# Kernel tuning notes

Hardware: AMD Instinct MI355X
Metric: run time of the kernel (lower is better)

## Reference

```python
import jax, jax.numpy as jnp
import numpy as np

N_NODES = 50000
N_EDGES = 800000
N_FEAT = 256
HIDDEN = 64
N_CLASSES = 16
T_END = 3.0  # opt['time']; rk4 takes one step over [0, 3]


def spline_conv(x, src, dst, p, W, R, b, n):
    """SplineConv, dim=1, kernel_size=2, degree=1 open B-spline, aggr='mean'.
    x: [n, Cin]; src/dst: [E]; p: [E,1] pseudo-coords in [0,1];
    W: [2, Cin, Cout]; R: [Cin, Cout]; b: [Cout]."""
    xj = x[src]  # gather source node features [E, Cin]
    # basis weights for K=2, degree=1: (1-p) on kernel 0, p on kernel 1
    msg = ((1.0 - p) * xj) @ W[0] + (p * xj) @ W[1]  # [E, Cout]
    agg = jax.ops.segment_sum(msg, dst, num_segments=n)
    deg = jax.ops.segment_sum(jnp.ones((msg.shape[0], 1), msg.dtype), dst, num_segments=n)
    return agg / jnp.maximum(deg, 1.0) + x @ R + b


def setup_inputs() -> dict:
    key = jax.random.key(0)
    ks = jax.random.split(key, 20)
    x = jax.random.normal(ks[0], (N_NODES, N_FEAT), jnp.float32)
    edge_attr = jax.random.uniform(ks[1], (N_EDGES, 1), jnp.float32)
    src = jax.random.randint(ks[2], (N_EDGES,), 0, N_NODES)
    dst = jax.random.randint(ks[3], (N_EDGES,), 0, N_NODES)

    def w(k, shape, fan_in):
        s = 1.0 / np.sqrt(fan_in)
        return jax.random.uniform(k, shape, jnp.float32, -s, s)

    # conv1: num_features -> hidden
    W1 = w(ks[4], (2, N_FEAT, HIDDEN), N_FEAT)
    R1 = w(ks[5], (N_FEAT, HIDDEN), N_FEAT)
    b1 = jnp.zeros((HIDDEN,), jnp.float32)
    # ODE func: two stacked SplineConvs hidden -> hidden
    Wa = w(ks[6], (2, HIDDEN, HIDDEN), HIDDEN)
    Ra = w(ks[7], (HIDDEN, HIDDEN), HIDDEN)
    ba = jnp.zeros((HIDDEN,), jnp.float32)
    Wb = w(ks[8], (2, HIDDEN, HIDDEN), HIDDEN)
    Rb = w(ks[9], (HIDDEN, HIDDEN), HIDDEN)
    bb = jnp.zeros((HIDDEN,), jnp.float32)
    # conv2: hidden -> num_classes
    W2 = w(ks[10], (2, HIDDEN, N_CLASSES), HIDDEN)
    R2 = w(ks[11], (HIDDEN, N_CLASSES), HIDDEN)
    b2 = jnp.zeros((N_CLASSES,), jnp.float32)

    return dict(x=x, edge_attr=edge_attr, src=src, dst=dst,
                W1=W1, R1=R1, b1=b1, Wa=Wa, Ra=Ra, ba=ba,
                Wb=Wb, Rb=Rb, bb=bb, W2=W2, R2=R2, b2=b2)


def reference(x, edge_attr, src, dst, W1, R1, b1, Wa, Ra, ba, Wb, Rb, bb, W2, R2, b2):
    n = x.shape[0]
    p = edge_attr
    h = jnp.tanh(spline_conv(x, src, dst, p, W1, R1, b1, n))
    # dropout is identity in eval mode

    def f(y):  # GCNLayer: two stacked SplineConvs, no activation
        y = spline_conv(y, src, dst, p, Wa, Ra, ba, n)
        return spline_conv(y, src, dst, p, Wb, Rb, bb, n)

    # single RK4 step from t=0 to t=T_END (torchdiffeq fixed-grid rk4 on s_span=[0,3])
    k1 = f(h)
    k2 = f(h + 0.5 * T_END * k1)
    k3 = f(h + 0.5 * T_END * k2)
    k4 = f(h + T_END * k3)
    h = h + (T_END / 6.0) * (k1 + 2.0 * k2 + 2.0 * k3 + k4)

    out = jnp.tanh(spline_conv(h, src, dst, p, W2, R2, b2, n))
    return jax.nn.log_softmax(out, axis=1)
```

## Files before the change

### kernel.cpp

```cpp
#include <hip/hip_runtime.h>
#include <math.h>

static inline int ceil_div(int a, int b) { return (a + b - 1) / b; }


__global__ __launch_bounds__(256) void zero2(int* __restrict__ a, int* __restrict__ b,
                                             int n) {
    int i = blockIdx.x * 256 + threadIdx.x;
    if (i < n) { a[i] = 0; b[i] = 0; }
}

__global__ __launch_bounds__(256) void hist_kernel(const int* __restrict__ dst,
                                                   int* __restrict__ deg, int E) {
    int e = blockIdx.x * 256 + threadIdx.x;
    if (e < E) atomicAdd(&deg[dst[e]], 1);
}

__global__ __launch_bounds__(256) void scan_blocksum(const int* __restrict__ deg,
                                                     int* __restrict__ bsum, int n) {
    __shared__ int red[256];
    int t = threadIdx.x;
    int base = blockIdx.x * 2048 + t * 8;
    int s = 0;
    #pragma unroll
    for (int i = 0; i < 8; ++i) {
        int idx = base + i;
        if (idx < n) s += deg[idx];
    }
    red[t] = s;
    __syncthreads();
    #pragma unroll
    for (int off = 128; off >= 1; off >>= 1) {
        if (t < off) red[t] += red[t + off];
        __syncthreads();
    }
    if (t == 0) bsum[blockIdx.x] = red[0];
}

__global__ __launch_bounds__(256) void scan_tops(int* __restrict__ bsum, int nb) {
    __shared__ int sh[256];
    int t = threadIdx.x;
    int orig = (t < nb) ? bsum[t] : 0;
    sh[t] = orig;
    __syncthreads();
    for (int off = 1; off < 256; off <<= 1) {
        int add = (t >= off) ? sh[t - off] : 0;
        __syncthreads();
        sh[t] += add;
        __syncthreads();
    }
    if (t < nb) bsum[t] = sh[t] - orig;
}

__global__ __launch_bounds__(256) void scan_final(const int* __restrict__ deg,
                                                  const int* __restrict__ bsum,
                                                  int* __restrict__ rowp,
                                                  float* __restrict__ invd,
                                                  int n, int E) {
    __shared__ int sh[256];
    int t = threadIdx.x;
    int base = blockIdx.x * 2048 + t * 8;
    int loc[8];
    int s = 0;
    #pragma unroll
    for (int i = 0; i < 8; ++i) {
        int idx = base + i;
        int d = (idx < n) ? deg[idx] : 0;
        loc[i] = d;
        s += d;
    }
    sh[t] = s;
    __syncthreads();
    for (int off = 1; off < 256; off <<= 1) {
        int add = (t >= off) ? sh[t - off] : 0;
        __syncthreads();
        sh[t] += add;
        __syncthreads();
    }
    int run = bsum[blockIdx.x] + (sh[t] - s);
    #pragma unroll
    for (int i = 0; i < 8; ++i) {
        int idx = base + i;
        if (idx < n) {
            rowp[idx] = run;
            int d = loc[i];
            run += d;
            invd[idx] = 1.0f / (float)(d > 1 ? d : 1);
        }
    }
    if (blockIdx.x == 0 && t == 0) rowp[n] = E;
}

__global__ __launch_bounds__(256) void scatter_idx(const int* __restrict__ dst,
                                                   const int* __restrict__ rowp,
                                                   int* __restrict__ fill,
                                                   int* __restrict__ ei, int E) {
    int e = blockIdx.x * 256 + threadIdx.x;
    if (e >= E) return;
    int d = dst[e];
    int pos = rowp[d] + atomicAdd(&fill[d], 1);
    ei[pos] = e;
}

__global__ __launch_bounds__(256) void sort_fill(const int* __restrict__ rowp,
                                                 int* __restrict__ ei,
                                                 const int* __restrict__ src,
                                                 const float* __restrict__ p,
                                                 int2* __restrict__ epk, int n) {
    int node = blockIdx.x * 256 + threadIdx.x;
    if (node >= n) return;
    int b = rowp[node], e = rowp[node + 1];
    for (int i = b + 1; i < e; ++i) {
        int key = ei[i];
        int j = i - 1;
        while (j >= b && ei[j] > key) { ei[j + 1] = ei[j]; --j; }
        ei[j + 1] = key;
    }
    for (int i = b; i < e; ++i) {
        int id = ei[i];
        epk[i] = make_int2(src[id], __float_as_int(p[id]));
    }
}

__global__ __launch_bounds__(256) void pack_all(
    const float* __restrict__ W1, const float* __restrict__ R1,
    const float* __restrict__ Wa, const float* __restrict__ Ra,
    const float* __restrict__ Wb, const float* __restrict__ Rb,
    const float* __restrict__ W2, const float* __restrict__ R2,
    float* __restrict__ Bc1, float* __restrict__ Bca,
    float* __restrict__ Bcb, float* __restrict__ Bc2) {
    int idx = blockIdx.x * 256 + threadIdx.x;
    const int S1 = 256 * 192, S2 = 192 * 64, S4 = 64 * 48;
    if (idx < S1) {
        int k = idx / 192, c = idx % 192;
        float v;
        if (c < 64)       v = W1[k * 64 + c];
        else if (c < 128) v = W1[256 * 64 + k * 64 + (c - 64)];
        else              v = R1[k * 64 + (c - 128)];
        Bc1[idx] = v;
        return;
    }
    idx -= S1;
    if (idx < S2) { Bca[idx] = (idx < 8192) ? Wa[idx] : Ra[idx - 8192]; return; }
    idx -= S2;
    if (idx < S2) { Bcb[idx] = (idx < 8192) ? Wb[idx] : Rb[idx - 8192]; return; }
    idx -= S2;
    if (idx < S4) {
        int k = idx / 48, c = idx % 48;
        float v;
        if (c < 16)      v = W2[k * 16 + c];
        else if (c < 32) v = W2[64 * 16 + k * 16 + (c - 16)];
        else             v = R2[k * 16 + (c - 32)];
        Bc2[idx] = v;
    }
}

__global__ __launch_bounds__(256) void edge_agg64_v5(const float* __restrict__ x,
                                                     const int* __restrict__ rowp,
                                                     const int2* __restrict__ epk,
                                                     const float* __restrict__ invd,
                                                     float* __restrict__ agg, int n) {
    int gid = blockIdx.x * 256 + threadIdx.x;
    int node = gid >> 4;
    if (node >= n) return;
    int c4 = (gid & 15) << 2;
    int e = rowp[node], eend = rowp[node + 1];
    float sx = 0.f, sy = 0.f, sz = 0.f, sw = 0.f;
    float px = 0.f, py = 0.f, pz = 0.f, pw = 0.f;
    for (; e + 4 <= eend; e += 4) {
        int2 q0 = epk[e], q1 = epk[e + 1], q2 = epk[e + 2], q3 = epk[e + 3];
        int s0 = q0.x, s1 = q1.x, s2 = q2.x, s3 = q3.x;
        float p0 = __int_as_float(q0.y), p1 = __int_as_float(q1.y);
        float p2 = __int_as_float(q2.y), p3 = __int_as_float(q3.y);
        float4 v0 = *reinterpret_cast<const float4*>(&x[(size_t)s0 * 64 + c4]);
        float4 v1 = *reinterpret_cast<const float4*>(&x[(size_t)s1 * 64 + c4]);
        float4 v2 = *reinterpret_cast<const float4*>(&x[(size_t)s2 * 64 + c4]);
        float4 v3 = *reinterpret_cast<const float4*>(&x[(size_t)s3 * 64 + c4]);
        sx += (v0.x + v1.x) + (v2.x + v3.x);
        sy += (v0.y + v1.y) + (v2.y + v3.y);
        sz += (v0.z + v1.z) + (v2.z + v3.z);
        sw += (v0.w + v1.w) + (v2.w + v3.w);
        px = fmaf(p0, v0.x, fmaf(p1, v1.x, fmaf(p2, v2.x, fmaf(p3, v3.x, px))));
        py = fmaf(p0, v0.y, fmaf(p1, v1.y, fmaf(p2, v2.y, fmaf(p3, v3.y, py))));
        pz = fmaf(p0, v0.z, fmaf(p1, v1.z, fmaf(p2, v2.z, fmaf(p3, v3.z, pz))));
        pw = fmaf(p0, v0.w, fmaf(p1, v1.w, fmaf(p2, v2.w, fmaf(p3, v3.w, pw))));
    }
    for (; e < eend; ++e) {
        int2 q = epk[e];
        int s = q.x;
        float pe = __int_as_float(q.y);
        float4 v = *reinterpret_cast<const float4*>(&x[(size_t)s * 64 + c4]);
        sx += v.x; sy += v.y; sz += v.z; sw += v.w;
        px = fmaf(pe, v.x, px); py = fmaf(pe, v.y, py);
        pz = fmaf(pe, v.z, pz); pw = fmaf(pe, v.w, pw);
    }
    float w = invd[node];
    float4 a0 = make_float4((sx - px) * w, (sy - py) * w, (sz - pz) * w, (sw - pw) * w);
    float4 a1 = make_float4(px * w, py * w, pz * w, pw * w);
    *reinterpret_cast<float4*>(&agg[(size_t)node * 128 + c4]) = a0;
    *reinterpret_cast<float4*>(&agg[(size_t)node * 128 + 64 + c4]) = a1;
}

__global__ __launch_bounds__(256) void hidden_gemm_db(
    const float* __restrict__ agg, const float* __restrict__ in,
    const float* __restrict__ B, const float* __restrict__ bias,
    int n, int mode, float* __restrict__ u_out,
    const float* __restrict__ hbuf, const float* __restrict__ acc_in,
    float* __restrict__ acc_out, float* __restrict__ t_out,
    float c1, float c2, float c3) {
    __shared__ __align__(16) float As[2][16][68];
    __shared__ __align__(16) float Bs[2][16][68];
    const int t = threadIdx.x;
    const int row0 = blockIdx.x * 64;
    const int ty = t >> 4, tx = t & 15;
    const int lrow = t >> 2, lk = (t & 3) << 2;
    const int bkk = t >> 4, bcol = (t & 15) << 2;

    float4 av = make_float4(0.f, 0.f, 0.f, 0.f);
    {
        int r = row0 + lrow;
        if (r < n) av = *reinterpret_cast<const float4*>(&agg[(size_t)r * 128 + lk]);
    }
    float4 bv = *reinterpret_cast<const float4*>(&B[(size_t)bkk * 64 + bcol]);
    As[0][lk + 0][lrow] = av.x; As[0][lk + 1][lrow] = av.y;
    As[0][lk + 2][lrow] = av.z; As[0][lk + 3][lrow] = av.w;
    *reinterpret_cast<float4*>(&Bs[0][bkk][bcol]) = bv;
    __syncthreads();

    float acc[4][4];
    #pragma unroll
    for (int i = 0; i < 4; ++i)
        #pragma unroll
        for (int j = 0; j < 4; ++j) acc[i][j] = 0.f;

    for (int kt = 0; kt < 12; ++kt) {
        const int cur = kt & 1;
        if (kt + 1 < 12) {
            int k0 = (kt + 1) << 4;
            int r = row0 + lrow;
            int kk = k0 + lk;
            av = make_float4(0.f, 0.f, 0.f, 0.f);
            if (r < n)
                av = (kk < 128)
                    ? *reinterpret_cast<const float4*>(&agg[(size_t)r * 128 + kk])
                    : *reinterpret_cast<const float4*>(&in[(size_t)r * 64 + (kk - 128)]);
            bv = *reinterpret_cast<const float4*>(&B[(size_t)(k0 + bkk) * 64 + bcol]);
        }
        #pragma unroll
        for (int kk = 0; kk < 16; ++kk) {
            float4 a4 = *reinterpret_cast<const float4*>(&As[cur][kk][ty << 2]);
            float4 b4 = *reinterpret_cast<const float4*>(&Bs[cur][kk][tx << 2]);
            float aa[4] = {a4.x, a4.y, a4.z, a4.w};
            float bb[4] = {b4.x, b4.y, b4.z, b4.w};
            #pragma unroll
            for (int i = 0; i < 4; ++i)
                #pragma unroll
                for (int j = 0; j < 4; ++j)
                    acc[i][j] = fmaf(aa[i], bb[j], acc[i][j]);
        }
        if (kt + 1 < 12) {
            const int nx = cur ^ 1;
            As[nx][lk + 0][lrow] = av.x; As[nx][lk + 1][lrow] = av.y;
            As[nx][lk + 2][lrow] = av.z; As[nx][lk + 3][lrow] = av.w;
            *reinterpret_cast<float4*>(&Bs[nx][bkk][bcol]) = bv;
        }
        __syncthreads();
    }

    float4 bia = *reinterpret_cast<const float4*>(&bias[tx << 2]);
    #pragma unroll
    for (int i = 0; i < 4; ++i) {
        int r = row0 + (ty << 2) + i;
        if (r >= n) continue;
        size_t idx = (size_t)r * 64 + (tx << 2);
        float4 v = make_float4(acc[i][0] + bia.x, acc[i][1] + bia.y,
                               acc[i][2] + bia.z, acc[i][3] + bia.w);
        if (mode == 0) {
            *reinterpret_cast<float4*>(&u_out[idx]) = v;
        } else {
            float4 ai = make_float4(0.f, 0.f, 0.f, 0.f);
            if (acc_in) ai = *reinterpret_cast<const float4*>(&acc_in[idx]);
            float4 an = make_float4(ai.x + c3 * v.x, ai.y + c3 * v.y,
                                    ai.z + c3 * v.z, ai.w + c3 * v.w);
            *reinterpret_cast<float4*>(&acc_out[idx]) = an;
            float4 hb = *reinterpret_cast<const float4*>(&hbuf[idx]);
            float4 to = make_float4(hb.x + c1 * v.x + c2 * an.x,
                                    hb.y + c1 * v.y + c2 * an.y,
                                    hb.z + c1 * v.z + c2 * an.z,
                                    hb.w + c1 * v.w + c2 * an.w);
            *reinterpret_cast<float4*>(&t_out[idx]) = to;
        }
    }
}

__global__ __launch_bounds__(128) void conv1_gemm_v5(const float* __restrict__ x,
                                                     const float* __restrict__ B,
                                                     int n, float* __restrict__ yz,
                                                     float* __restrict__ base,
                                                     const float* __restrict__ b1) {
    __shared__ __align__(16) float As[16][36];
    __shared__ __align__(16) float Bs[16][200];
    const int t = threadIdx.x;
    const int row0 = blockIdx.x * 32;
    const int ty = t >> 4, tx = t & 15;
    const int arow = t >> 2, alk = (t & 3) << 2;
    const int bkk0 = t >> 4, bcol = (t & 15) << 2;
    float acc[4][12];
    #pragma unroll
    for (int i = 0; i < 4; ++i)
        #pragma unroll
        for (int j = 0; j < 12; ++j) acc[i][j] = 0.f;

    for (int kt = 0; kt < 16; ++kt) {
        int k0 = kt << 4;
        {
            float4 av = make_float4(0.f, 0.f, 0.f, 0.f);
            int r = row0 + arow;
            if (r < n)
                av = *reinterpret_cast<const float4*>(&x[(size_t)r * 256 + k0 + alk]);
            As[alk + 0][arow] = av.x; As[alk + 1][arow] = av.y;
            As[alk + 2][arow] = av.z; As[alk + 3][arow] = av.w;
        }
        #pragma unroll
        for (int hh = 0; hh < 2; ++hh) {
            int kk = bkk0 + 8 * hh;
            const float* bp = &B[(size_t)(k0 + kk) * 192 + bcol];
            *reinterpret_cast<float4*>(&Bs[kk][bcol])       = *reinterpret_cast<const float4*>(bp);
            *reinterpret_cast<float4*>(&Bs[kk][bcol + 64])  = *reinterpret_cast<const float4*>(bp + 64);
            *reinterpret_cast<float4*>(&Bs[kk][bcol + 128]) = *reinterpret_cast<const float4*>(bp + 128);
        }
        __syncthreads();
        #pragma unroll
        for (int kk = 0; kk < 16; ++kk) {
            float4 a0 = *reinterpret_cast<const float4*>(&As[kk][ty << 2]);
            float4 b0 = *reinterpret_cast<const float4*>(&Bs[kk][tx << 2]);
            float4 b1q = *reinterpret_cast<const float4*>(&Bs[kk][(tx << 2) + 64]);
            float4 b2q = *reinterpret_cast<const float4*>(&Bs[kk][(tx << 2) + 128]);
            float aa[4] = {a0.x, a0.y, a0.z, a0.w};
            float bb[12] = {b0.x, b0.y, b0.z, b0.w, b1q.x, b1q.y, b1q.z, b1q.w,
                            b2q.x, b2q.y, b2q.z, b2q.w};
            #pragma unroll
            for (int i = 0; i < 4; ++i)
                #pragma unroll
                for (int j = 0; j < 12; ++j)
                    acc[i][j] = fmaf(aa[i], bb[j], acc[i][j]);
        }
        __syncthreads();
    }

    float4 bb4 = *reinterpret_cast<const float4*>(&b1[tx << 2]);
    #pragma unroll
    for (int i = 0; i < 4; ++i) {
        int r = row0 + (ty << 2) + i;
        if (r >= n) continue;
        float4 q0 = make_float4(acc[i][0], acc[i][1], acc[i][2], acc[i][3]);
        float4 q1 = make_float4(acc[i][4], acc[i][5], acc[i][6], acc[i][7]);
        float4 q2 = make_float4(acc[i][8] + bb4.x, acc[i][9] + bb4.y,
                                acc[i][10] + bb4.z, acc[i][11] + bb4.w);
        *reinterpret_cast<float4*>(&yz[(size_t)r * 128 + (tx << 2)]) = q0;
        *reinterpret_cast<float4*>(&yz[(size_t)r * 128 + 64 + (tx << 2)]) = q1;
        *reinterpret_cast<float4*>(&base[(size_t)r * 64 + (tx << 2)]) = q2;
    }
}

__global__ __launch_bounds__(256) void edge_tf64_v8(const float* __restrict__ yz,
                                                    const int* __restrict__ rowp,
                                                    const int2* __restrict__ epk,
                                                    const float* __restrict__ invd,
                                                    const float* __restrict__ base,
                                                    float* __restrict__ out, int n) {
    int gid = blockIdx.x * 256 + threadIdx.x;
    int node = gid >> 3;
    if (node >= n) return;
    int c8 = (gid & 7) << 3;
    int e = rowp[node], eend = rowp[node + 1];
    float a[8] = {0.f, 0.f, 0.f, 0.f, 0.f, 0.f, 0.f, 0.f};
    for (; e + 2 <= eend; e += 2) {
        int2 q0 = epk[e], q1 = epk[e + 1];
        int s0 = q0.x, s1 = q1.x;
        float p0 = __int_as_float(q0.y), p1 = __int_as_float(q1.y);
        float4 y0a = *reinterpret_cast<const float4*>(&yz[(size_t)s0 * 128 + c8]);
        float4 y0b = *reinterpret_cast<const float4*>(&yz[(size_t)s0 * 128 + c8 + 4]);
        float4 z0a = *reinterpret_cast<const float4*>(&yz[(size_t)s0 * 128 + 64 + c8]);
        float4 z0b = *reinterpret_cast<const float4*>(&yz[(size_t)s0 * 128 + 64 + c8 + 4]);
        float4 y1a = *reinterpret_cast<const float4*>(&yz[(size_t)s1 * 128 + c8]);
        float4 y1b = *reinterpret_cast<const float4*>(&yz[(size_t)s1 * 128 + c8 + 4]);
        float4 z1a = *reinterpret_cast<const float4*>(&yz[(size_t)s1 * 128 + 64 + c8]);
        float4 z1b = *reinterpret_cast<const float4*>(&yz[(size_t)s1 * 128 + 64 + c8 + 4]);
        const float* ya0 = &y0a.x; const float* yb0 = &y0b.x;
        const float* za0 = &z0a.x; const float* zb0 = &z0b.x;
        const float* ya1 = &y1a.x; const float* yb1 = &y1b.x;
        const float* za1 = &z1a.x; const float* zb1 = &z1b.x;
        #pragma unroll
        for (int j = 0; j < 4; ++j) {
            a[j]     += fmaf(p0, za0[j] - ya0[j], ya0[j]) + fmaf(p1, za1[j] - ya1[j], ya1[j]);
            a[4 + j] += fmaf(p0, zb0[j] - yb0[j], yb0[j]) + fmaf(p1, zb1[j] - yb1[j], yb1[j]);
        }
    }
    for (; e < eend; ++e) {
        int2 q = epk[e];
        int s = q.x;
        float pe = __int_as_float(q.y);
        float4 ya = *reinterpret_cast<const float4*>(&yz[(size_t)s * 128 + c8]);
        float4 yb = *reinterpret_cast<const float4*>(&yz[(size_t)s * 128 + c8 + 4]);
        float4 za = *reinterpret_cast<const float4*>(&yz[(size_t)s * 128 + 64 + c8]);
        float4 zb = *reinterpret_cast<const float4*>(&yz[(size_t)s * 128 + 64 + c8 + 4]);
        const float* fy = &ya.x; const float* gy = &yb.x;
        const float* fz = &za.x; const float* gz = &zb.x;
        #pragma unroll
        for (int j = 0; j < 4; ++j) {
            a[j]     += fmaf(pe, fz[j] - fy[j], fy[j]);
            a[4 + j] += fmaf(pe, gz[j] - gy[j], gy[j]);
        }
    }
    float w = invd[node];
    size_t idx = (size_t)node * 64 + c8;
    float4 ba = *reinterpret_cast<const float4*>(&base[idx]);
    float4 bbv = *reinterpret_cast<const float4*>(&base[idx + 4]);
    float4 o0 = make_float4(tanhf(fmaf(a[0], w, ba.x)), tanhf(fmaf(a[1], w, ba.y)),
                            tanhf(fmaf(a[2], w, ba.z)), tanhf(fmaf(a[3], w, ba.w)));
    float4 o1 = make_float4(tanhf(fmaf(a[4], w, bbv.x)), tanhf(fmaf(a[5], w, bbv.y)),
                            tanhf(fmaf(a[6], w, bbv.z)), tanhf(fmaf(a[7], w, bbv.w)));
    *reinterpret_cast<float4*>(&out[idx]) = o0;
    *reinterpret_cast<float4*>(&out[idx + 4]) = o1;
}

__global__ __launch_bounds__(256) void edge_tf16_lsm(const float* __restrict__ yz,
                                                     const int* __restrict__ rowp,
                                                     const int2* __restrict__ epk,
                                                     const float* __restrict__ invd,
                                                     const float* __restrict__ base,
                                                     float* __restrict__ out, int n) {
    int gid = blockIdx.x * 256 + threadIdx.x;
    int node = gid >> 4;
    if (node >= n) return;
    int c = gid & 15;
    int e = rowp[node], eend = rowp[node + 1];
    float a = 0.f;
    for (; e + 4 <= eend; e += 4) {
        int2 q0 = epk[e], q1 = epk[e + 1], q2 = epk[e + 2], q3 = epk[e + 3];
        int s0 = q0.x, s1 = q1.x, s2 = q2.x, s3 = q3.x;
        float p0 = __int_as_float(q0.y), p1 = __int_as_float(q1.y);
        float p2 = __int_as_float(q2.y), p3 = __int_as_float(q3.y);
        float y0 = yz[(size_t)s0 * 32 + c],      z0 = yz[(size_t)s0 * 32 + 16 + c];
        float y1 = yz[(size_t)s1 * 32 + c],      z1 = yz[(size_t)s1 * 32 + 16 + c];
        float y2 = yz[(size_t)s2 * 32 + c],      z2 = yz[(size_t)s2 * 32 + 16 + c];
        float y3 = yz[(size_t)s3 * 32 + c],      z3 = yz[(size_t)s3 * 32 + 16 + c];
        a += fmaf(p0, z0 - y0, y0);
        a += fmaf(p1, z1 - y1, y1);
        a += fmaf(p2, z2 - y2, y2);
        a += fmaf(p3, z3 - y3, y3);
    }
    for (; e < eend; ++e) {
        int2 q = epk[e];
        int s = q.x; float pe = __int_as_float(q.y);
        float y = yz[(size_t)s * 32 + c], z = yz[(size_t)s * 32 + 16 + c];
        a += fmaf(pe, z - y, y);
    }
    float o = tanhf(a * invd[node] + base[(size_t)node * 16 + c]);
    float m = o;
    #pragma unroll
    for (int off = 8; off >= 1; off >>= 1) m = fmaxf(m, __shfl_xor(m, off, 16));
    float ex = expf(o - m);
    float s = ex;
    #pragma unroll
    for (int off = 8; off >= 1; off >>= 1) s += __shfl_xor(s, off, 16);
    out[(size_t)node * 16 + c] = (o - m) - logf(s);
}

__global__ __launch_bounds__(256) void gemm_tiled(
    const float* __restrict__ A0, int lda0, int K0,
    const float* __restrict__ A1, int lda1,
    const float* __restrict__ B,
    int n, int K, int M,
    float* __restrict__ out0, int w0, const float* __restrict__ bias0,
    float* __restrict__ out1, int w1, const float* __restrict__ bias1,
    int split) {
    __shared__ __align__(16) float As[16][68];
    __shared__ __align__(16) float Bs[16][68];
    const int t = threadIdx.x;
    const int row0 = blockIdx.x * 64;
    const int col0 = blockIdx.y * 64;
    const int ty = t >> 4, tx = t & 15;
    const int lrow = t >> 2, lk = (t & 3) << 2;
    const int bkk = t >> 4, bcol = (t & 15) << 2;
    float acc[4][4];
    #pragma unroll
    for (int i = 0; i < 4; ++i)
        #pragma unroll
        for (int j = 0; j < 4; ++j) acc[i][j] = 0.f;

    for (int k0 = 0; k0 < K; k0 += 16) {
        float4 av = make_float4(0.f, 0.f, 0.f, 0.f);
        {
            int r = row0 + lrow;
            if (r < n) {
                int kk = k0 + lk;
                const float* src = (kk < K0)
                    ? (A0 + (size_t)r * lda0 + kk)
                    : (A1 + (size_t)r * lda1 + (kk - K0));
                av = *reinterpret_cast<const float4*>(src);
            }
        }
        float4 bv = make_float4(0.f, 0.f, 0.f, 0.f);
        {
            int c = col0 + bcol;
            int kk = k0 + bkk;
            if (c < M) bv = *reinterpret_cast<const float4*>(B + (size_t)kk * M + c);
        }
        As[lk + 0][lrow] = av.x; As[lk + 1][lrow] = av.y;
        As[lk + 2][lrow] = av.z; As[lk + 3][lrow] = av.w;
        *reinterpret_cast<float4*>(&Bs[bkk][bcol]) = bv;
        __syncthreads();
        #pragma unroll
        for (int kk = 0; kk < 16; ++kk) {
            float4 a4 = *reinterpret_cast<const float4*>(&As[kk][ty << 2]);
            float4 b4 = *reinterpret_cast<const float4*>(&Bs[kk][tx << 2]);
            float aa[4] = {a4.x, a4.y, a4.z, a4.w};
            float bb[4] = {b4.x, b4.y, b4.z, b4.w};
            #pragma unroll
            for (int i = 0; i < 4; ++i)
                #pragma unroll
                for (int j = 0; j < 4; ++j)
                    acc[i][j] = fmaf(aa[i], bb[j], acc[i][j]);
        }
        __syncthreads();
    }

    #pragma unroll
    for (int i = 0; i < 4; ++i) {
        int r = row0 + (ty << 2) + i;
        if (r >= n) continue;
        #pragma unroll
        for (int j = 0; j < 4; ++j) {
            int c = col0 + (tx << 2) + j;
            if (c >= M) continue;
            float v = acc[i][j];
            if (c < split) {
                if (bias0) v += bias0[c];
                out0[(size_t)r * w0 + c] = v;
            } else {
                int cc = c - split;
                if (bias1) v += bias1[cc];
                out1[(size_t)r * w1 + cc] = v;
            }
        }
    }
}


static void hidden_conv(hipStream_t stream, const float* in, float* agg,
                        const int* rowp, const int2* epk,
                        const float* invd, const float* Bc, const float* bias, int n,
                        int mode, float* u_out,
                        const float* h, const float* acc_in, float* acc_out,
                        float* t_out, float c1, float c2, float c3) {
    edge_agg64_v5<<<ceil_div(n * 16, 256), 256, 0, stream>>>(in, rowp, epk, invd,
                                                             agg, n);
    hidden_gemm_db<<<ceil_div(n, 64), 256, 0, stream>>>(agg, in, Bc, bias, n, mode,
                                                        u_out, h, acc_in, acc_out,
                                                        t_out, c1, c2, c3);
}

extern "C" void kernel_launch(void* const* d_in, const int* in_sizes, int n_in,
                              void* d_out, int out_size, void* d_ws, size_t ws_size,
                              hipStream_t stream) {
    const float* x  = (const float*)d_in[0];
    const float* pE = (const float*)d_in[1];
    const int*   sr = (const int*)d_in[2];
    const int*   ds = (const int*)d_in[3];
    const float* W1 = (const float*)d_in[4];
    const float* R1 = (const float*)d_in[5];
    const float* b1 = (const float*)d_in[6];
    const float* Wa = (const float*)d_in[7];
    const float* Ra = (const float*)d_in[8];
    const float* ba = (const float*)d_in[9];
    const float* Wb = (const float*)d_in[10];
    const float* Rb = (const float*)d_in[11];
    const float* bb = (const float*)d_in[12];
    const float* W2 = (const float*)d_in[13];
    const float* R2 = (const float*)d_in[14];
    const float* b2 = (const float*)d_in[15];
    const int n = in_sizes[0] / 256;
    const int E = in_sizes[2];
    float* out = (float*)d_out;

    char* w = (char*)d_ws;
    auto alloc = [&](size_t bytes) -> void* {
        void* ptr = (void*)w;
        w += (bytes + 255) & ~(size_t)255;
        return ptr;
    };
    int nscan = ceil_div(n, 2048);
    int*   deg  = (int*)alloc((size_t)n * 4);
    int*   fill = (int*)alloc((size_t)n * 4);
    int*   rowp = (int*)alloc((size_t)(n + 1) * 4);
    float* invd = (float*)alloc((size_t)n * 4);
    int*   bsum = (int*)alloc((size_t)256 * 4);
    int*   ei   = (int*)alloc((size_t)E * 4);
    int2*  epk  = (int2*)alloc((size_t)E * 8);
    float* Bc1  = (float*)alloc((size_t)256 * 192 * 4);
    float* Bca  = (float*)alloc((size_t)192 * 64 * 4);
    float* Bcb  = (float*)alloc((size_t)192 * 64 * 4);
    float* Bc2  = (float*)alloc((size_t)64 * 48 * 4);
    float* big0 = (float*)alloc((size_t)n * 128 * 4);
    float* big1 = (float*)alloc((size_t)n * 64 * 4);
    float* h    = (float*)alloc((size_t)n * 64 * 4);
    float* u    = (float*)alloc((size_t)n * 64 * 4);
    float* tb   = (float*)alloc((size_t)n * 64 * 4);
    float* acc  = (float*)alloc((size_t)n * 64 * 4);

    const int PACK_TOTAL = 256 * 192 + 2 * 192 * 64 + 64 * 48;

    zero2<<<ceil_div(n, 256), 256, 0, stream>>>(deg, fill, n);
    pack_all<<<ceil_div(PACK_TOTAL, 256), 256, 0, stream>>>(W1, R1, Wa, Ra, Wb, Rb,
                                                            W2, R2, Bc1, Bca, Bcb, Bc2);
    hist_kernel<<<ceil_div(E, 256), 256, 0, stream>>>(ds, deg, E);
    scan_blocksum<<<nscan, 256, 0, stream>>>(deg, bsum, n);
    scan_tops<<<1, 256, 0, stream>>>(bsum, nscan);
    scan_final<<<nscan, 256, 0, stream>>>(deg, bsum, rowp, invd, n, E);
    scatter_idx<<<ceil_div(E, 256), 256, 0, stream>>>(ds, rowp, fill, ei, E);
    sort_fill<<<ceil_div(n, 256), 256, 0, stream>>>(rowp, ei, sr, pE, epk, n);

    conv1_gemm_v5<<<ceil_div(n, 32), 128, 0, stream>>>(x, Bc1, n, big0, big1, b1);
    edge_tf64_v8<<<ceil_div(n * 8, 256), 256, 0, stream>>>(big0, rowp, epk, invd,
                                                           big1, h, n);

    hidden_conv(stream, h, big0, rowp, epk, invd, Bca, ba, n, 0, u,
                nullptr, nullptr, nullptr, nullptr, 0.f, 0.f, 0.f);
    hidden_conv(stream, u, big0, rowp, epk, invd, Bcb, bb, n, 1, nullptr,
                h, nullptr, acc, tb, 1.5f, 0.f, 1.f);
    hidden_conv(stream, tb, big0, rowp, epk, invd, Bca, ba, n, 0, u,
                nullptr, nullptr, nullptr, nullptr, 0.f, 0.f, 0.f);
    hidden_conv(stream, u, big0, rowp, epk, invd, Bcb, bb, n, 1, nullptr,
                h, acc, acc, tb, 1.5f, 0.f, 2.f);
    hidden_conv(stream, tb, big0, rowp, epk, invd, Bca, ba, n, 0, u,
                nullptr, nullptr, nullptr, nullptr, 0.f, 0.f, 0.f);
    hidden_conv(stream, u, big0, rowp, epk, invd, Bcb, bb, n, 1, nullptr,
                h, acc, acc, tb, 3.f, 0.f, 2.f);
    hidden_conv(stream, tb, big0, rowp, epk, invd, Bca, ba, n, 0, u,
                nullptr, nullptr, nullptr, nullptr, 0.f, 0.f, 0.f);
    hidden_conv(stream, u, big0, rowp, epk, invd, Bcb, bb, n, 1, nullptr,
                h, acc, acc, tb, 0.f, 0.5f, 1.f);

    gemm_tiled<<<dim3(ceil_div(n, 64), 1), 256, 0, stream>>>(
        tb, 64, 64, nullptr, 0, Bc2, n, 64, 48,
        big0, 32, nullptr, big1, 16, b2, 32);
    edge_tf16_lsm<<<ceil_div(n * 16, 256), 256, 0, stream>>>(big0, rowp, epk, invd,
                                                             big1, out, n);
}
```

Measured before the change: 894.9 us.

## Fuse hidden-layer edge aggregation into GEMM kernel via shared-memory staging

Merges the separate edge-aggregation kernel and the hidden GEMM into one kernel. Each block first gathers neighbour features for its 64 nodes, writing the transposed aggregates into shared memory, then runs the GEMM against those and the self features. This removes the global write and re-read of the 128-wide aggregate buffer and one launch per conv, and unrolls the gather loop to 8 edges. In exchange the GEMM loses its double buffering, shared memory per block grows (about 39 KB), which may cut occupancy, and the gather parallelism per block drops to 16 nodes at a time.

```diff
diff --git a/kernel.cpp b/kernel.cpp
--- a/kernel.cpp
+++ b/kernel.cpp
@@ -155,78 +155,104 @@
     }
 }
 
-__global__ __launch_bounds__(256) void edge_agg64_v5(const float* __restrict__ x,
-                                                     const int* __restrict__ rowp,
-                                                     const int2* __restrict__ epk,
-                                                     const float* __restrict__ invd,
-                                                     float* __restrict__ agg, int n) {
-    int gid = blockIdx.x * 256 + threadIdx.x;
-    int node = gid >> 4;
-    if (node >= n) return;
-    int c4 = (gid & 15) << 2;
-    int e = rowp[node], eend = rowp[node + 1];
-    float sx = 0.f, sy = 0.f, sz = 0.f, sw = 0.f;
-    float px = 0.f, py = 0.f, pz = 0.f, pw = 0.f;
-    for (; e + 4 <= eend; e += 4) {
-        int2 q0 = epk[e], q1 = epk[e + 1], q2 = epk[e + 2], q3 = epk[e + 3];
-        int s0 = q0.x, s1 = q1.x, s2 = q2.x, s3 = q3.x;
-        float p0 = __int_as_float(q0.y), p1 = __int_as_float(q1.y);
-        float p2 = __int_as_float(q2.y), p3 = __int_as_float(q3.y);
-        float4 v0 = *reinterpret_cast<const float4*>(&x[(size_t)s0 * 64 + c4]);
-        float4 v1 = *reinterpret_cast<const float4*>(&x[(size_t)s1 * 64 + c4]);
-        float4 v2 = *reinterpret_cast<const float4*>(&x[(size_t)s2 * 64 + c4]);
-        float4 v3 = *reinterpret_cast<const float4*>(&x[(size_t)s3 * 64 + c4]);
-        sx += (v0.x + v1.x) + (v2.x + v3.x);
-        sy += (v0.y + v1.y) + (v2.y + v3.y);
-        sz += (v0.z + v1.z) + (v2.z + v3.z);
-        sw += (v0.w + v1.w) + (v2.w + v3.w);
-        px = fmaf(p0, v0.x, fmaf(p1, v1.x, fmaf(p2, v2.x, fmaf(p3, v3.x, px))));
-        py = fmaf(p0, v0.y, fmaf(p1, v1.y, fmaf(p2, v2.y, fmaf(p3, v3.y, py))));
-        pz = fmaf(p0, v0.z, fmaf(p1, v1.z, fmaf(p2, v2.z, fmaf(p3, v3.z, pz))));
-        pw = fmaf(p0, v0.w, fmaf(p1, v1.w, fmaf(p2, v2.w, fmaf(p3, v3.w, pw))));
-    }
-    for (; e < eend; ++e) {
-        int2 q = epk[e];
-        int s = q.x;
-        float pe = __int_as_float(q.y);
-        float4 v = *reinterpret_cast<const float4*>(&x[(size_t)s * 64 + c4]);
-        sx += v.x; sy += v.y; sz += v.z; sw += v.w;
-        px = fmaf(pe, v.x, px); py = fmaf(pe, v.y, py);
-        pz = fmaf(pe, v.z, pz); pw = fmaf(pe, v.w, pw);
-    }
-    float w = invd[node];
-    float4 a0 = make_float4((sx - px) * w, (sy - py) * w, (sz - pz) * w, (sw - pw) * w);
-    float4 a1 = make_float4(px * w, py * w, pz * w, pw * w);
-    *reinterpret_cast<float4*>(&agg[(size_t)node * 128 + c4]) = a0;
-    *reinterpret_cast<float4*>(&agg[(size_t)node * 128 + 64 + c4]) = a1;
-}
-
-__global__ __launch_bounds__(256) void hidden_gemm_db(
-    const float* __restrict__ agg, const float* __restrict__ in,
+__global__ __launch_bounds__(256) void hidden_fused(
+    const float* __restrict__ in, const int* __restrict__ rowp,
+    const int2* __restrict__ epk, const float* __restrict__ invd,
     const float* __restrict__ B, const float* __restrict__ bias,
     int n, int mode, float* __restrict__ u_out,
     const float* __restrict__ hbuf, const float* __restrict__ acc_in,
     float* __restrict__ acc_out, float* __restrict__ t_out,
     float c1, float c2, float c3) {
-    __shared__ __align__(16) float As[2][16][68];
-    __shared__ __align__(16) float Bs[2][16][68];
+    __shared__ __align__(16) float Ag[128][68];
+    __shared__ __align__(16) float Bs[16][68];
     const int t = threadIdx.x;
     const int row0 = blockIdx.x * 64;
+
+    const int c4 = (t & 15) << 2;
+    const int ng = t >> 4;
+    #pragma unroll 1
+    for (int b = 0; b < 4; ++b) {
+        int nl = b * 16 + ng;
+        int node = row0 + nl;
+        float sx = 0.f, sy = 0.f, sz = 0.f, sw = 0.f;
+        float px = 0.f, py = 0.f, pz = 0.f, pw = 0.f;
+        if (node < n) {
+            int e = rowp[node], eend = rowp[node + 1];
+            for (; e + 8 <= eend; e += 8) {
+                int2 q[8];
+                #pragma unroll
+                for (int i = 0; i < 8; ++i) q[i] = epk[e + i];
+                float4 v[8];
+                #pragma unroll
+                for (int i = 0; i < 8; ++i)
+                    v[i] = *reinterpret_cast<const float4*>(
+                        &in[(size_t)q[i].x * 64 + c4]);
+                #pragma unroll
+                for (int g = 0; g < 2; ++g) {
+                    float4 v0 = v[4 * g], v1 = v[4 * g + 1];
+                    float4 v2 = v[4 * g + 2], v3 = v[4 * g + 3];
+                    float p0 = __int_as_float(q[4 * g].y);
+                    float p1 = __int_as_float(q[4 * g + 1].y);
+                    float p2 = __int_as_float(q[4 * g + 2].y);
+                    float p3 = __int_as_float(q[4 * g + 3].y);
+                    sx += (v0.x + v1.x) + (v2.x + v3.x);
+                    sy += (v0.y + v1.y) + (v2.y + v3.y);
+                    sz += (v0.z + v1.z) + (v2.z + v3.z);
+                    sw += (v0.w + v1.w) + (v2.w + v3.w);
+                    px = fmaf(p0, v0.x, fmaf(p1, v1.x, fmaf(p2, v2.x, fmaf(p3, v3.x, px))));
+                    py = fmaf(p0, v0.y, fmaf(p1, v1.y, fmaf(p2, v2.y, fmaf(p3, v3.y, py))));
+                    pz = fmaf(p0, v0.z, fmaf(p1, v1.z, fmaf(p2, v2.z, fmaf(p3, v3.z, pz))));
+                    pw = fmaf(p0, v0.w, fmaf(p1, v1.w, fmaf(p2, v2.w, fmaf(p3, v3.w, pw))));
+                }
+            }
+            for (; e + 4 <= eend; e += 4) {
+                int2 q0 = epk[e], q1 = epk[e + 1], q2 = epk[e + 2], q3 = epk[e + 3];
+                int s0 = q0.x, s1 = q1.x, s2 = q2.x, s3 = q3.x;
+                float p0 = __int_as_float(q0.y), p1 = __int_as_float(q1.y);
+                float p2 = __int_as_float(q2.y), p3 = __int_as_float(q3.y);
+                float4 v0 = *reinterpret_cast<const float4*>(&in[(size_t)s0 * 64 + c4]);
+                float4 v1 = *reinterpret_cast<const float4*>(&in[(size_t)s1 * 64 + c4]);
+                float4 v2 = *reinterpret_cast<const float4*>(&in[(size_t)s2 * 64 + c4]);
+                float4 v3 = *reinterpret_cast<const float4*>(&in[(size_t)s3 * 64 + c4]);
+                sx += (v0.x + v1.x) + (v2.x + v3.x);
+                sy += (v0.y + v1.y) + (v2.y + v3.y);
+                sz += (v0.z + v1.z) + (v2.z + v3.z);
+                sw += (v0.w + v1.w) + (v2.w + v3.w);
+                px = fmaf(p0, v0.x, fmaf(p1, v1.x, fmaf(p2, v2.x, fmaf(p3, v3.x, px))));
+                py = fmaf(p0, v0.y, fmaf(p1, v1.y, fmaf(p2, v2.y, fmaf(p3, v3.y, py))));
+                pz = fmaf(p0, v0.z, fmaf(p1, v1.z, fmaf(p2, v2.z, fmaf(p3, v3.z, pz))));
+                pw = fmaf(p0, v0.w, fmaf(p1, v1.w, fmaf(p2, v2.w, fmaf(p3, v3.w, pw))));
+            }
+            for (; e < eend; ++e) {
+                int2 q = epk[e];
+                int s = q.x;
+                float pe = __int_as_float(q.y);
+                float4 v = *reinterpret_cast<const float4*>(&in[(size_t)s * 64 + c4]);
+                sx += v.x; sy += v.y; sz += v.z; sw += v.w;
+                px = fmaf(pe, v.x, px); py = fmaf(pe, v.y, py);
+                pz = fmaf(pe, v.z, pz); pw = fmaf(pe, v.w, pw);
+            }
+            float w = invd[node];
+            Ag[c4 + 0][nl] = (sx - px) * w;
+            Ag[c4 + 1][nl] = (sy - py) * w;
+            Ag[c4 + 2][nl] = (sz - pz) * w;
+            Ag[c4 + 3][nl] = (sw - pw) * w;
+            Ag[64 + c4 + 0][nl] = px * w;
+            Ag[64 + c4 + 1][nl] = py * w;
+            Ag[64 + c4 + 2][nl] = pz * w;
+            Ag[64 + c4 + 3][nl] = pw * w;
+        } else {
+            Ag[c4 + 0][nl] = 0.f; Ag[c4 + 1][nl] = 0.f;
+            Ag[c4 + 2][nl] = 0.f; Ag[c4 + 3][nl] = 0.f;
+            Ag[64 + c4 + 0][nl] = 0.f; Ag[64 + c4 + 1][nl] = 0.f;
+            Ag[64 + c4 + 2][nl] = 0.f; Ag[64 + c4 + 3][nl] = 0.f;
+        }
+    }
+    __syncthreads();
+
     const int ty = t >> 4, tx = t & 15;
+    const int bkk = t >> 4, bcol = (t & 15) << 2;
     const int lrow = t >> 2, lk = (t & 3) << 2;
-    const int bkk = t >> 4, bcol = (t & 15) << 2;
-
-    float4 av = make_float4(0.f, 0.f, 0.f, 0.f);
-    {
-        int r = row0 + lrow;
-        if (r < n) av = *reinterpret_cast<const float4*>(&agg[(size_t)r * 128 + lk]);
-    }
-    float4 bv = *reinterpret_cast<const float4*>(&B[(size_t)bkk * 64 + bcol]);
-    As[0][lk + 0][lrow] = av.x; As[0][lk + 1][lrow] = av.y;
-    As[0][lk + 2][lrow] = av.z; As[0][lk + 3][lrow] = av.w;
-    *reinterpret_cast<float4*>(&Bs[0][bkk][bcol]) = bv;
-    __syncthreads();
-
     float acc[4][4];
     #pragma unroll
     for (int i = 0; i < 4; ++i)
@@ -234,22 +260,24 @@
         for (int j = 0; j < 4; ++j) acc[i][j] = 0.f;
 
     for (int kt = 0; kt < 12; ++kt) {
-        const int cur = kt & 1;
-        if (kt + 1 < 12) {
-            int k0 = (kt + 1) << 4;
+        *reinterpret_cast<float4*>(&Bs[bkk][bcol]) =
+            *reinterpret_cast<const float4*>(&B[(size_t)(kt * 16 + bkk) * 64 + bcol]);
+        if (kt >= 8) {
             int r = row0 + lrow;
-            int kk = k0 + lk;
-            av = make_float4(0.f, 0.f, 0.f, 0.f);
+            float4 av = make_float4(0.f, 0.f, 0.f, 0.f);
             if (r < n)
-                av = (kk < 128)
-                    ? *reinterpret_cast<const float4*>(&agg[(size_t)r * 128 + kk])
-                    : *reinterpret_cast<const float4*>(&in[(size_t)r * 64 + (kk - 128)]);
-            bv = *reinterpret_cast<const float4*>(&B[(size_t)(k0 + bkk) * 64 + bcol]);
-        }
+                av = *reinterpret_cast<const float4*>(
+                    &in[(size_t)r * 64 + (kt - 8) * 16 + lk]);
+            int kb = (kt - 8) * 16 + lk;
+            Ag[kb + 0][lrow] = av.x; Ag[kb + 1][lrow] = av.y;
+            Ag[kb + 2][lrow] = av.z; Ag[kb + 3][lrow] = av.w;
+        }
+        __syncthreads();
+        const int ab = (kt < 8) ? kt * 16 : (kt - 8) * 16;
         #pragma unroll
         for (int kk = 0; kk < 16; ++kk) {
-            float4 a4 = *reinterpret_cast<const float4*>(&As[cur][kk][ty << 2]);
-            float4 b4 = *reinterpret_cast<const float4*>(&Bs[cur][kk][tx << 2]);
+            float4 a4 = *reinterpret_cast<const float4*>(&Ag[ab + kk][ty << 2]);
+            float4 b4 = *reinterpret_cast<const float4*>(&Bs[kk][tx << 2]);
             float aa[4] = {a4.x, a4.y, a4.z, a4.w};
             float bb[4] = {b4.x, b4.y, b4.z, b4.w};
             #pragma unroll
@@ -257,12 +285,6 @@
                 #pragma unroll
                 for (int j = 0; j < 4; ++j)
                     acc[i][j] = fmaf(aa[i], bb[j], acc[i][j]);
-        }
-        if (kt + 1 < 12) {
-            const int nx = cur ^ 1;
-            As[nx][lk + 0][lrow] = av.x; As[nx][lk + 1][lrow] = av.y;
-            As[nx][lk + 2][lrow] = av.z; As[nx][lk + 3][lrow] = av.w;
-            *reinterpret_cast<float4*>(&Bs[nx][bkk][bcol]) = bv;
         }
         __syncthreads();
     }
@@ -549,17 +571,15 @@
 }
 
 
-static void hidden_conv(hipStream_t stream, const float* in, float* agg,
+static void hidden_conv(hipStream_t stream, const float* in,
                         const int* rowp, const int2* epk,
                         const float* invd, const float* Bc, const float* bias, int n,
                         int mode, float* u_out,
                         const float* h, const float* acc_in, float* acc_out,
                         float* t_out, float c1, float c2, float c3) {
-    edge_agg64_v5<<<ceil_div(n * 16, 256), 256, 0, stream>>>(in, rowp, epk, invd,
-                                                             agg, n);
-    hidden_gemm_db<<<ceil_div(n, 64), 256, 0, stream>>>(agg, in, Bc, bias, n, mode,
-                                                        u_out, h, acc_in, acc_out,
-                                                        t_out, c1, c2, c3);
+    hidden_fused<<<ceil_div(n, 64), 256, 0, stream>>>(in, rowp, epk, invd, Bc, bias,
+                                                      n, mode, u_out, h, acc_in,
+                                                      acc_out, t_out, c1, c2, c3);
 }
 
 extern "C" void kernel_launch(void* const* d_in, const int* in_sizes, int n_in,
@@ -626,21 +646,21 @@
     edge_tf64_v8<<<ceil_div(n * 8, 256), 256, 0, stream>>>(big0, rowp, epk, invd,
                                                            big1, h, n);
 
-    hidden_conv(stream, h, big0, rowp, epk, invd, Bca, ba, n, 0, u,
+    hidden_conv(stream, h, rowp, epk, invd, Bca, ba, n, 0, u,
                 nullptr, nullptr, nullptr, nullptr, 0.f, 0.f, 0.f);
-    hidden_conv(stream, u, big0, rowp, epk, invd, Bcb, bb, n, 1, nullptr,
+    hidden_conv(stream, u, rowp, epk, invd, Bcb, bb, n, 1, nullptr,
                 h, nullptr, acc, tb, 1.5f, 0.f, 1.f);
-    hidden_conv(stream, tb, big0, rowp, epk, invd, Bca, ba, n, 0, u,
+    hidden_conv(stream, tb, rowp, epk, invd, Bca, ba, n, 0, u,
                 nullptr, nullptr, nullptr, nullptr, 0.f, 0.f, 0.f);
-    hidden_conv(stream, u, big0, rowp, epk, invd, Bcb, bb, n, 1, nullptr,
+    hidden_conv(stream, u, rowp, epk, invd, Bcb, bb, n, 1, nullptr,
                 h, acc, acc, tb, 1.5f, 0.f, 2.f);
-    hidden_conv(stream, tb, big0, rowp, epk, invd, Bca, ba, n, 0, u,
+    hidden_conv(stream, tb, rowp, epk, invd, Bca, ba, n, 0, u,
                 nullptr, nullptr, nullptr, nullptr, 0.f, 0.f, 0.f);
-    hidden_conv(stream, u, big0, rowp, epk, invd, Bcb, bb, n, 1, nullptr,
+    hidden_conv(stream, u, rowp, epk, invd, Bcb, bb, n, 1, nullptr,
                 h, acc, acc, tb, 3.f, 0.f, 2.f);
-    hidden_conv(stream, tb, big0, rowp, epk, invd, Bca, ba, n, 0, u,
+    hidden_conv(stream, tb, rowp, epk, invd, Bca, ba, n, 0, u,
                 nullptr, nullptr, nullptr, nullptr, 0.f, 0.f, 0.f);
-    hidden_conv(stream, u, big0, rowp, epk, invd, Bcb, bb, n, 1, nullptr,
+    hidden_conv(stream, u, rowp, epk, invd, Bcb, bb, n, 1, nullptr,
                 h, acc, acc, tb, 0.f, 0.5f, 1.f);
 
     gemm_tiled<<<dim3(ceil_div(n, 64), 1), 256, 0, stream>>>(
```

Result: slower. 956.1 us (+6.8%).

## Process nodes in degree-sorted order in edge aggregation kernels

Applied to the files above, without the earlier changes.

Adds a counting sort of nodes by in-degree (bins capped at 63) that builds a permutation, and the edge aggregation kernels now pick their node through this permutation. Nodes with similar degree then share a wavefront, which is meant to reduce divergence in the per-edge loops. In exchange the node feature reads and output writes follow permuted, non-contiguous order, and the setup gains four extra small kernel launches.

```diff
diff --git a/kernel.cpp b/kernel.cpp
--- a/kernel.cpp
+++ b/kernel.cpp
@@ -119,6 +119,45 @@
     for (int i = b; i < e; ++i) {
         int id = ei[i];
         epk[i] = make_int2(src[id], __float_as_int(p[id]));
+    }
+}
+
+__global__ __launch_bounds__(64) void bins_zero(int* __restrict__ bins) {
+    bins[threadIdx.x] = 0;
+}
+
+__global__ __launch_bounds__(256) void bins_count(const int* __restrict__ deg,
+                                                  int* __restrict__ bins, int n) {
+    int i = blockIdx.x * 256 + threadIdx.x;
+    if (i < n) {
+        int d = deg[i];
+        if (d > 63) d = 63;
+        atomicAdd(&bins[d], 1);
+    }
+}
+
+__global__ __launch_bounds__(64) void bins_scan(int* __restrict__ bins) {
+    __shared__ int sh[64];
+    int t = threadIdx.x;
+    sh[t] = bins[t];
+    __syncthreads();
+    if (t == 0) {
+        int run = 0;
+        for (int i = 0; i < 64; ++i) { int c = sh[i]; sh[i] = run; run += c; }
+    }
+    __syncthreads();
+    bins[t] = sh[t];
+}
+
+__global__ __launch_bounds__(256) void perm_fill(const int* __restrict__ deg,
+                                                 int* __restrict__ bins,
+                                                 int* __restrict__ perm, int n) {
+    int i = blockIdx.x * 256 + threadIdx.x;
+    if (i < n) {
+        int d = deg[i];
+        if (d > 63) d = 63;
+        int pos = atomicAdd(&bins[d], 1);
+        perm[pos] = i;
     }
 }
 
@@ -159,10 +198,12 @@
                                                      const int* __restrict__ rowp,
                                                      const int2* __restrict__ epk,
                                                      const float* __restrict__ invd,
+                                                     const int* __restrict__ perm,
                                                      float* __restrict__ agg, int n) {
     int gid = blockIdx.x * 256 + threadIdx.x;
-    int node = gid >> 4;
-    if (node >= n) return;
+    int pi = gid >> 4;
+    if (pi >= n) return;
+    int node = perm[pi];
     int c4 = (gid & 15) << 2;
     int e = rowp[node], eend = rowp[node + 1];
     float sx = 0.f, sy = 0.f, sz = 0.f, sw = 0.f;
@@ -367,11 +408,13 @@
                                                     const int* __restrict__ rowp,
                                                     const int2* __restrict__ epk,
                                                     const float* __restrict__ invd,
+                                                    const int* __restrict__ perm,
                                                     const float* __restrict__ base,
                                                     float* __restrict__ out, int n) {
     int gid = blockIdx.x * 256 + threadIdx.x;
-    int node = gid >> 3;
-    if (node >= n) return;
+    int pi = gid >> 3;
+    if (pi >= n) return;
+    int node = perm[pi];
     int c8 = (gid & 7) << 3;
     int e = rowp[node], eend = rowp[node + 1];
     float a[8] = {0.f, 0.f, 0.f, 0.f, 0.f, 0.f, 0.f, 0.f};
@@ -429,11 +472,13 @@
                                                      const int* __restrict__ rowp,
                                                      const int2* __restrict__ epk,
                                                      const float* __restrict__ invd,
+                                                     const int* __restrict__ perm,
                                                      const float* __restrict__ base,
                                                      float* __restrict__ out, int n) {
     int gid = blockIdx.x * 256 + threadIdx.x;
-    int node = gid >> 4;
-    if (node >= n) return;
+    int pi = gid >> 4;
+    if (pi >= n) return;
+    int node = perm[pi];
     int c = gid & 15;
     int e = rowp[node], eend = rowp[node + 1];
     float a = 0.f;
@@ -551,12 +596,13 @@
 
 static void hidden_conv(hipStream_t stream, const float* in, float* agg,
                         const int* rowp, const int2* epk,
-                        const float* invd, const float* Bc, const float* bias, int n,
+                        const float* invd, const int* perm,
+                        const float* Bc, const float* bias, int n,
                         int mode, float* u_out,
                         const float* h, const float* acc_in, float* acc_out,
                         float* t_out, float c1, float c2, float c3) {
     edge_agg64_v5<<<ceil_div(n * 16, 256), 256, 0, stream>>>(in, rowp, epk, invd,
-                                                             agg, n);
+                                                             perm, agg, n);
     hidden_gemm_db<<<ceil_div(n, 64), 256, 0, stream>>>(agg, in, Bc, bias, n, mode,
                                                         u_out, h, acc_in, acc_out,
                                                         t_out, c1, c2, c3);
@@ -597,6 +643,8 @@
     int*   rowp = (int*)alloc((size_t)(n + 1) * 4);
     float* invd = (float*)alloc((size_t)n * 4);
     int*   bsum = (int*)alloc((size_t)256 * 4);
+    int*   bins = (int*)alloc((size_t)64 * 4);
+    int*   perm = (int*)alloc((size_t)n * 4);
     int*   ei   = (int*)alloc((size_t)E * 4);
     int2*  epk  = (int2*)alloc((size_t)E * 8);
     float* Bc1  = (float*)alloc((size_t)256 * 192 * 4);
@@ -613,39 +661,43 @@
     const int PACK_TOTAL = 256 * 192 + 2 * 192 * 64 + 64 * 48;
 
     zero2<<<ceil_div(n, 256), 256, 0, stream>>>(deg, fill, n);
+    bins_zero<<<1, 64, 0, stream>>>(bins);
     pack_all<<<ceil_div(PACK_TOTAL, 256), 256, 0, stream>>>(W1, R1, Wa, Ra, Wb, Rb,
                                                             W2, R2, Bc1, Bca, Bcb, Bc2);
     hist_kernel<<<ceil_div(E, 256), 256, 0, stream>>>(ds, deg, E);
     scan_blocksum<<<nscan, 256, 0, stream>>>(deg, bsum, n);
     scan_tops<<<1, 256, 0, stream>>>(bsum, nscan);
     scan_final<<<nscan, 256, 0, stream>>>(deg, bsum, rowp, invd, n, E);
+    bins_count<<<ceil_div(n, 256), 256, 0, stream>>>(deg, bins, n);
+    bins_scan<<<1, 64, 0, stream>>>(bins);
+    perm_fill<<<ceil_div(n, 256), 256, 0, stream>>>(deg, bins, perm, n);
     scatter_idx<<<ceil_div(E, 256), 256, 0, stream>>>(ds, rowp, fill, ei, E);
     sort_fill<<<ceil_div(n, 256), 256, 0, stream>>>(rowp, ei, sr, pE, epk, n);
 
     conv1_gemm_v5<<<ceil_div(n, 32), 128, 0, stream>>>(x, Bc1, n, big0, big1, b1);
     edge_tf64_v8<<<ceil_div(n * 8, 256), 256, 0, stream>>>(big0, rowp, epk, invd,
-                                                           big1, h, n);
-
-    hidden_conv(stream, h, big0, rowp, epk, invd, Bca, ba, n, 0, u,
+                                                           perm, big1, h, n);
+
+    hidden_conv(stream, h, big0, rowp, epk, invd, perm, Bca, ba, n, 0, u,
                 nullptr, nullptr, nullptr, nullptr, 0.f, 0.f, 0.f);
-    hidden_conv(stream, u, big0, rowp, epk, invd, Bcb, bb, n, 1, nullptr,
+    hidden_conv(stream, u, big0, rowp, epk, invd, perm, Bcb, bb, n, 1, nullptr,
                 h, nullptr, acc, tb, 1.5f, 0.f, 1.f);
-    hidden_conv(stream, tb, big0, rowp, epk, invd, Bca, ba, n, 0, u,
+    hidden_conv(stream, tb, big0, rowp, epk, invd, perm, Bca, ba, n, 0, u,
                 nullptr, nullptr, nullptr, nullptr, 0.f, 0.f, 0.f);
-    hidden_conv(stream, u, big0, rowp, epk, invd, Bcb, bb, n, 1, nullptr,
+    hidden_conv(stream, u, big0, rowp, epk, invd, perm, Bcb, bb, n, 1, nullptr,
                 h, acc, acc, tb, 1.5f, 0.f, 2.f);
-    hidden_conv(stream, tb, big0, rowp, epk, invd, Bca, ba, n, 0, u,
+    hidden_conv(stream, tb, big0, rowp, epk, invd, perm, Bca, ba, n, 0, u,
                 nullptr, nullptr, nullptr, nullptr, 0.f, 0.f, 0.f);
-    hidden_conv(stream, u, big0, rowp, epk, invd, Bcb, bb, n, 1, nullptr,
+    hidden_conv(stream, u, big0, rowp, epk, invd, perm, Bcb, bb, n, 1, nullptr,
                 h, acc, acc, tb, 3.f, 0.f, 2.f);
-    hidden_conv(stream, tb, big0, rowp, epk, invd, Bca, ba, n, 0, u,
+    hidden_conv(stream, tb, big0, rowp, epk, invd, perm, Bca, ba, n, 0, u,
                 nullptr, nullptr, nullptr, nullptr, 0.f, 0.f, 0.f);
-    hidden_conv(stream, u, big0, rowp, epk, invd, Bcb, bb, n, 1, nullptr,
+    hidden_conv(stream, u, big0, rowp, epk, invd, perm, Bcb, bb, n, 1, nullptr,
                 h, acc, acc, tb, 0.f, 0.5f, 1.f);
 
     gemm_tiled<<<dim3(ceil_div(n, 64), 1), 256, 0, stream>>>(
         tb, 64, 64, nullptr, 0, Bc2, n, 64, 48,
         big0, 32, nullptr, big1, 16, b2, 32);
     edge_tf16_lsm<<<ceil_div(n * 16, 256), 256, 0, stream>>>(big0, rowp, epk, invd,
-                                                             big1, out, n);
-}
+                                                             perm, big1, out, n);
+}
```

Result: slower. 1.163 ms (+30.0%).
